# Optimization experiments

Hardware: AMD Instinct MI355X
Metric: run time of the kernel (lower is better)

## Reference

```python
import jax, jax.numpy as jnp
import numpy as np

NTOKENS = 50257
NHID = 1024
NPC = int(np.ceil(np.sqrt(NTOKENS)))            # 225 tokens per class
NCLASSES = int(np.ceil(NTOKENS / NPC))          # 224 classes
BATCH = 1024
INITRANGE = 0.1


def setup_inputs() -> dict:
    key = jax.random.key(0)
    k1, k2, k3, k4 = jax.random.split(key, 4)
    inputs = jax.random.normal(k1, (BATCH, NHID), dtype=jnp.float32)
    labels = jax.random.randint(k2, (BATCH,), 0, NTOKENS, dtype=jnp.int64)
    layer_top_W = jax.random.uniform(k3, (NHID, NCLASSES), minval=-INITRANGE, maxval=INITRANGE, dtype=jnp.float32)
    layer_top_b = jnp.zeros((NCLASSES,), dtype=jnp.float32)
    layer_bottom_W = jax.random.uniform(k4, (NCLASSES, NHID, NPC), minval=-INITRANGE, maxval=INITRANGE, dtype=jnp.float32)
    layer_bottom_b = jnp.zeros((NCLASSES, NPC), dtype=jnp.float32)
    return {
        "inputs": inputs,
        "labels": labels,
        "layer_top_W": layer_top_W,
        "layer_top_b": layer_top_b,
        "layer_bottom_W": layer_bottom_W,
        "layer_bottom_b": layer_bottom_b,
    }


def reference(inputs, labels, layer_top_W, layer_top_b, layer_bottom_W, layer_bottom_b):
    batch_size = inputs.shape[0]
    # decompose label into (class, within-class) position; old-torch `/` on Long == floor div
    pos_top = labels // NPC            # [B]
    pos_bottom = labels % NPC          # [B]

    # top-level class distribution: [B, nclasses]
    top_logits = inputs @ layer_top_W + layer_top_b
    top_probs = jax.nn.softmax(top_logits, axis=1)

    # gather per-sample class weight slices and do batched matvec:
    # layer_bottom_W[pos_top]: [B, nhid, npc]
    bottom_logits = jnp.einsum("bd,bdc->bc", inputs, layer_bottom_W[pos_top]) + layer_bottom_b[pos_top]
    bottom_probs = jax.nn.softmax(bottom_logits, axis=1)

    rows = jnp.arange(batch_size)
    target_probs = top_probs[rows, pos_top] * bottom_probs[rows, pos_bottom]  # [B]
    return target_probs
```

## Files before the change

### kernel.cpp

```cpp
#include <hip/hip_runtime.h>
#include <math.h>

#define NHID 1024
#define NPC  225
#define NCLS 224
#define BATCH 1024

#define MAX_ITEMS 352
#define N_TOP     (BATCH / 8)
#define GRID_SZ   (1 + N_TOP + MAX_ITEMS)

#define WS_NITEMS 0
#define WS_ORDER  16
#define WS_ITEMS  2048
#define WS_PTOP   4096
#define WS_DONE   6144

#define NITEMS_TAG 0x5A5A0000
#define DONE_MAGIC 0x5A5A5A5A

__device__ __forceinline__ void st_rlx(int* p, int v) {
    __hip_atomic_store(p, v, __ATOMIC_RELAXED, __HIP_MEMORY_SCOPE_AGENT);
}
__device__ __forceinline__ int ld_rlx(int* p) {
    return __hip_atomic_load(p, __ATOMIC_RELAXED, __HIP_MEMORY_SCOPE_AGENT);
}

__global__ __launch_bounds__(512, 4) void hs_fused(
    const float* __restrict__ X, const int* __restrict__ labels,
    const float* __restrict__ Wt, const float* __restrict__ bt,
    const float* __restrict__ Wb, const float* __restrict__ bb,
    int* __restrict__ ws, float* __restrict__ out)
{
    __shared__ __align__(16) float sm[12288];
    __shared__ int s_n;
    const int tid  = threadIdx.x;
    const int bid  = blockIdx.x;
    const int wave = tid >> 6;
    const int lane = tid & 63;

    if (bid == 0) {
        int* cnt   = (int*)sm;
        int* scan  = (int*)sm + 256;
        int* iscan = (int*)sm + 512;
        int* cur   = (int*)sm + 768;
        if (tid < 256) cnt[tid] = 0;
        __syncthreads();
        for (int i = tid; i < BATCH; i += 512)
            atomicAdd(&cnt[labels[i] / NPC], 1);
        __syncthreads();
        int myc = 0, myi = 0;
        if (tid < 256) {
            myc = (tid < NCLS) ? cnt[tid] : 0;
            myi = (myc + 7) >> 3;
            scan[tid] = myc; iscan[tid] = myi;
        }
        __syncthreads();
        for (int off = 1; off < 256; off <<= 1) {
            int a = 0, b = 0;
            if (tid < 256 && tid >= off) { a = scan[tid - off]; b = iscan[tid - off]; }
            __syncthreads();
            if (tid < 256) { scan[tid] += a; iscan[tid] += b; }
            __syncthreads();
        }
        if (tid < 256) {
            const int sbase = scan[tid] - myc;
            const int ibase = iscan[tid] - myi;
            cur[tid] = sbase;
            if (tid < NCLS) {
                for (int t = 0; t < myi; ++t) {
                    int* it = ws + WS_ITEMS + 4 * (ibase + t);
                    st_rlx(it + 0, tid);
                    st_rlx(it + 1, sbase + 8 * t);
                    st_rlx(it + 2, min(8, myc - 8 * t));
                }
            }
        }
        __syncthreads();
        for (int i = tid; i < BATCH; i += 512) {
            int c = labels[i] / NPC;
            int p = atomicAdd(&cur[c], 1);
            st_rlx(ws + WS_ORDER + p, i);
        }
        __syncthreads();
        if (tid == 0)
            __hip_atomic_store(ws + WS_NITEMS, NITEMS_TAG | iscan[255],
                               __ATOMIC_RELEASE, __HIP_MEMORY_SCOPE_AGENT);
        return;
    }

    if (bid <= N_TOP) {
        const int sbase = (bid - 1) * 8;
        for (int idx = tid; idx < 2048; idx += 512) {
            const int j  = idx >> 8;
            const int d4 = idx & 255;
            const float4 v = ((const float4*)&X[(size_t)(sbase + j) * NHID])[d4];
            sm[(4 * d4 + 0) * 12 + j] = v.x;
            sm[(4 * d4 + 1) * 12 + j] = v.y;
            sm[(4 * d4 + 2) * 12 + j] = v.z;
            sm[(4 * d4 + 3) * 12 + j] = v.w;
        }
        __syncthreads();

        float acc[8][4];
#pragma unroll
        for (int j = 0; j < 8; ++j)
#pragma unroll
            for (int k = 0; k < 4; ++k) acc[j][k] = 0.f;

        const int c0 = lane, c1 = lane + 64, c2 = lane + 128, c3 = lane + 192;
        const bool m3 = (c3 < NCLS);
        const int d0 = wave * 128;
        const float* Wr = Wt + (size_t)d0 * NCLS;

        auto ldrow = [&](int r, float* o) {
            const float* p = Wr + (size_t)r * NCLS;
            o[0] = p[c0]; o[1] = p[c1]; o[2] = p[c2];
            o[3] = m3 ? p[c3] : 0.f;
        };
        float wbuf[4][4];
        ldrow(0, wbuf[0]); ldrow(1, wbuf[1]); ldrow(2, wbuf[2]); ldrow(3, wbuf[3]);

#pragma unroll 4
        for (int dd = 0; dd < 128; ++dd) {
            const int slot = dd & 3;
            const float cw0 = wbuf[slot][0], cw1 = wbuf[slot][1],
                        cw2 = wbuf[slot][2], cw3 = wbuf[slot][3];
            ldrow(min(dd + 4, 127), wbuf[slot]);
            const float4 a = *(const float4*)&sm[(d0 + dd) * 12 + 0];
            const float4 b = *(const float4*)&sm[(d0 + dd) * 12 + 4];
            const float xi[8] = {a.x, a.y, a.z, a.w, b.x, b.y, b.z, b.w};
#pragma unroll
            for (int j = 0; j < 8; ++j) {
                acc[j][0] = fmaf(xi[j], cw0, acc[j][0]);
                acc[j][1] = fmaf(xi[j], cw1, acc[j][1]);
                acc[j][2] = fmaf(xi[j], cw2, acc[j][2]);
                acc[j][3] = fmaf(xi[j], cw3, acc[j][3]);
            }
        }
        __syncthreads();

        float* red = sm;
        if (wave >= 4) {
#pragma unroll
            for (int j = 0; j < 8; ++j)
#pragma unroll
                for (int k = 0; k < 4; ++k) {
                    int c = lane + 64 * k;
                    if (c < NCLS) red[((wave - 4) * 8 + j) * 232 + c] = acc[j][k];
                }
        }
        __syncthreads();
        if (wave < 4) {
#pragma unroll
            for (int j = 0; j < 8; ++j)
#pragma unroll
                for (int k = 0; k < 4; ++k) {
                    int c = lane + 64 * k;
                    if (c < NCLS) red[(wave * 8 + j) * 232 + c] += acc[j][k];
                }
        }
        __syncthreads();

        {
            const int j = wave;
            const int s = sbase + j;
            float v[4];
#pragma unroll
            for (int k = 0; k < 4; ++k) {
                int c = lane + 64 * k;
                v[k] = (c < NCLS)
                         ? (red[(0 * 8 + j) * 232 + c] + red[(1 * 8 + j) * 232 + c] +
                            red[(2 * 8 + j) * 232 + c] + red[(3 * 8 + j) * 232 + c] +
                            bt[c])
                         : -INFINITY;
            }
            float m = fmaxf(fmaxf(v[0], v[1]), fmaxf(v[2], v[3]));
            for (int o = 32; o > 0; o >>= 1) m = fmaxf(m, __shfl_xor(m, o));
            float e = expf(v[0] - m) + expf(v[1] - m) + expf(v[2] - m) + expf(v[3] - m);
            for (int o = 32; o > 0; o >>= 1) e += __shfl_xor(e, o);
            const int pt = labels[s] / NPC;
            if (lane == (pt & 63))
                st_rlx(ws + WS_PTOP + s, __float_as_int(expf(v[pt >> 6] - m) / e));
        }
        __syncthreads();
        if (tid == 0)
            __hip_atomic_store(ws + WS_DONE + (bid - 1), DONE_MAGIC,
                               __ATOMIC_RELEASE, __HIP_MEMORY_SCOPE_AGENT);
        return;
    }

    if (tid == 0) {
        int dv;
        for (;;) {
            dv = __hip_atomic_load(ws + WS_NITEMS, __ATOMIC_ACQUIRE,
                                   __HIP_MEMORY_SCOPE_AGENT);
            if ((dv & 0xFFFF0000) == NITEMS_TAG) break;
            __builtin_amdgcn_s_sleep(8);
        }
        s_n = dv & 0xFFFF;
    }
    __syncthreads();
    const int bi = bid - 1 - N_TOP;
    if (bi >= s_n) return;

    int* it = ws + WS_ITEMS + 4 * bi;
    const int cls = ld_rlx(it + 0);
    const int s0  = ld_rlx(it + 1);
    const int nt  = ld_rlx(it + 2);

    int s_ids[8];
#pragma unroll
    for (int j = 0; j < 8; ++j)
        s_ids[j] = (j < nt) ? ld_rlx(ws + WS_ORDER + s0 + j) : 0;

    for (int idx = tid; idx < 2048; idx += 512) {
        const int j  = idx >> 8;
        const int d4 = idx & 255;
        float4 v = make_float4(0.f, 0.f, 0.f, 0.f);
        if (j < nt) v = ((const float4*)&X[(size_t)s_ids[j] * NHID])[d4];
        sm[(4 * d4 + 0) * 12 + j] = v.x;
        sm[(4 * d4 + 1) * 12 + j] = v.y;
        sm[(4 * d4 + 2) * 12 + j] = v.z;
        sm[(4 * d4 + 3) * 12 + j] = v.w;
    }
    __syncthreads();

    float acc[8][4];
#pragma unroll
    for (int j = 0; j < 8; ++j)
#pragma unroll
        for (int k = 0; k < 4; ++k) acc[j][k] = 0.f;

    const int c0 = lane, c1 = lane + 64, c2 = lane + 128, c3 = lane + 192;
    const bool m3 = (c3 < NPC);
    const int d0 = wave * 128;
    const float* Wr = Wb + (size_t)cls * (NHID * NPC) + (size_t)d0 * NPC;

    auto ldrow = [&](int r, float* o) {
        const float* p = Wr + (size_t)r * NPC;
        o[0] = __builtin_nontemporal_load(p + c0);
        o[1] = __builtin_nontemporal_load(p + c1);
        o[2] = __builtin_nontemporal_load(p + c2);
        o[3] = m3 ? __builtin_nontemporal_load(p + c3) : 0.f;
    };
    float wbuf[4][4];
    ldrow(0, wbuf[0]); ldrow(1, wbuf[1]); ldrow(2, wbuf[2]); ldrow(3, wbuf[3]);

#pragma unroll 4
    for (int dd = 0; dd < 128; ++dd) {
        const int slot = dd & 3;
        const float cw0 = wbuf[slot][0], cw1 = wbuf[slot][1],
                    cw2 = wbuf[slot][2], cw3 = wbuf[slot][3];
        ldrow(min(dd + 4, 127), wbuf[slot]);
        const float4 a = *(const float4*)&sm[(d0 + dd) * 12 + 0];
        const float4 b = *(const float4*)&sm[(d0 + dd) * 12 + 4];
        const float xi[8] = {a.x, a.y, a.z, a.w, b.x, b.y, b.z, b.w};
#pragma unroll
        for (int j = 0; j < 8; ++j) {
            acc[j][0] = fmaf(xi[j], cw0, acc[j][0]);
            acc[j][1] = fmaf(xi[j], cw1, acc[j][1]);
            acc[j][2] = fmaf(xi[j], cw2, acc[j][2]);
            acc[j][3] = fmaf(xi[j], cw3, acc[j][3]);
        }
    }
    __syncthreads();

    float* red = sm;
    if (wave >= 4) {
#pragma unroll
        for (int j = 0; j < 8; ++j)
#pragma unroll
            for (int k = 0; k < 4; ++k) {
                int c = lane + 64 * k;
                if (c < NPC) red[((wave - 4) * 8 + j) * 232 + c] = acc[j][k];
            }
    }
    __syncthreads();
    if (wave < 4) {
#pragma unroll
        for (int j = 0; j < 8; ++j)
#pragma unroll
            for (int k = 0; k < 4; ++k) {
                int c = lane + 64 * k;
                if (c < NPC) red[(wave * 8 + j) * 232 + c] += acc[j][k];
            }
    }
    __syncthreads();

    {
        const int j = wave;
        if (j < nt) {
            const int s = s_ids[j];
            float v[4];
#pragma unroll
            for (int k = 0; k < 4; ++k) {
                int c = lane + 64 * k;
                v[k] = (c < NPC)
                         ? (red[(0 * 8 + j) * 232 + c] + red[(1 * 8 + j) * 232 + c] +
                            red[(2 * 8 + j) * 232 + c] + red[(3 * 8 + j) * 232 + c] +
                            bb[(size_t)cls * NPC + c])
                         : -INFINITY;
            }
            float m = fmaxf(fmaxf(v[0], v[1]), fmaxf(v[2], v[3]));
            for (int o = 32; o > 0; o >>= 1) m = fmaxf(m, __shfl_xor(m, o));
            float e = expf(v[0] - m) + expf(v[1] - m) + expf(v[2] - m) + expf(v[3] - m);
            for (int o = 32; o > 0; o >>= 1) e += __shfl_xor(e, o);
            const int pb = labels[s] % NPC;
            if (lane == (pb & 63)) {
                int dv;
                for (;;) {
                    dv = __hip_atomic_load(ws + WS_DONE + (s >> 3), __ATOMIC_ACQUIRE,
                                           __HIP_MEMORY_SCOPE_AGENT);
                    if (dv == DONE_MAGIC) break;
                    __builtin_amdgcn_s_sleep(8);
                }
                const float pt = __int_as_float(ld_rlx(ws + WS_PTOP + s));
                out[s] = pt * (expf(v[pb >> 6] - m) / e);
            }
        }
    }
}

extern "C" void kernel_launch(void* const* d_in, const int* in_sizes, int n_in,
                              void* d_out, int out_size, void* d_ws, size_t ws_size,
                              hipStream_t stream)
{
    const float* X      = (const float*)d_in[0];
    const int*   labels = (const int*)  d_in[1];
    const float* Wt     = (const float*)d_in[2];
    const float* bt     = (const float*)d_in[3];
    const float* Wb     = (const float*)d_in[4];
    const float* bb     = (const float*)d_in[5];

    hipLaunchKernelGGL(hs_fused, dim3(GRID_SZ), dim3(512), 0, stream,
                       X, labels, Wt, bt, Wb, bb, (int*)d_ws, (float*)d_out);
}
```

Measured before the change: 325.1 us.

## Split fused kernel into two launches and widen blocks to 1024 threads

Replaces the single persistent-style kernel, which used spin-wait flags between grouping, top-softmax and bottom blocks, with two stream-ordered kernels: one for grouping plus the top softmax, one for the bottom softmax. Blocks grow to 1024 threads, so each wave covers 64 hidden dims instead of 128, followed by an 8-way shared-memory reduction. The X transpose store pattern also changes. This removes the atomic polling and sleep loops, in exchange for a second launch and a hard barrier that stops the bottom work from overlapping with the top work.

```diff
diff --git a/kernel.cpp b/kernel.cpp
--- a/kernel.cpp
+++ b/kernel.cpp
@@ -8,221 +8,203 @@
 
 #define MAX_ITEMS 352
 #define N_TOP     (BATCH / 8)
-#define GRID_SZ   (1 + N_TOP + MAX_ITEMS)
 
 #define WS_NITEMS 0
 #define WS_ORDER  16
 #define WS_ITEMS  2048
 #define WS_PTOP   4096
-#define WS_DONE   6144
-
-#define NITEMS_TAG 0x5A5A0000
-#define DONE_MAGIC 0x5A5A5A5A
-
-__device__ __forceinline__ void st_rlx(int* p, int v) {
-    __hip_atomic_store(p, v, __ATOMIC_RELAXED, __HIP_MEMORY_SCOPE_AGENT);
+
+__device__ __forceinline__ void group_samples(const int* __restrict__ labels,
+                                              int* __restrict__ ws,
+                                              float* __restrict__ smf, int tid)
+{
+    int* cnt   = (int*)smf;
+    int* scan  = (int*)smf + 256;
+    int* iscan = (int*)smf + 512;
+    int* cur   = (int*)smf + 768;
+
+    if (tid < 256) cnt[tid] = 0;
+    __syncthreads();
+    for (int i = tid; i < BATCH; i += 1024)
+        atomicAdd(&cnt[labels[i] / NPC], 1);
+    __syncthreads();
+
+    int myc = 0, myi = 0;
+    if (tid < 256) {
+        myc = (tid < NCLS) ? cnt[tid] : 0;
+        myi = (myc + 7) >> 3;
+        scan[tid]  = myc;
+        iscan[tid] = myi;
+    }
+    __syncthreads();
+    for (int off = 1; off < 256; off <<= 1) {
+        int a = 0, b = 0;
+        if (tid < 256 && tid >= off) { a = scan[tid - off]; b = iscan[tid - off]; }
+        __syncthreads();
+        if (tid < 256) { scan[tid] += a; iscan[tid] += b; }
+        __syncthreads();
+    }
+    if (tid < 256) {
+        const int sbase = scan[tid]  - myc;
+        const int ibase = iscan[tid] - myi;
+        if (tid == 255) ws[WS_NITEMS] = iscan[255];
+        cur[tid] = sbase;
+        if (tid < NCLS) {
+            for (int t = 0; t < myi; ++t) {
+                int* it = ws + WS_ITEMS + 4 * (ibase + t);
+                it[0] = tid;
+                it[1] = sbase + 8 * t;
+                it[2] = min(8, myc - 8 * t);
+            }
+        }
+    }
+    __syncthreads();
+    for (int i = tid; i < BATCH; i += 1024) {
+        int c = labels[i] / NPC;
+        int p = atomicAdd(&cur[c], 1);
+        ws[WS_ORDER + p] = i;
+    }
 }
-__device__ __forceinline__ int ld_rlx(int* p) {
-    return __hip_atomic_load(p, __ATOMIC_RELAXED, __HIP_MEMORY_SCOPE_AGENT);
-}
-
-__global__ __launch_bounds__(512, 4) void hs_fused(
-    const float* __restrict__ X, const int* __restrict__ labels,
-    const float* __restrict__ Wt, const float* __restrict__ bt,
-    const float* __restrict__ Wb, const float* __restrict__ bb,
-    int* __restrict__ ws, float* __restrict__ out)
+
+__global__ __launch_bounds__(1024, 4) void k1_top(const float* __restrict__ X,
+                                                  const int* __restrict__ labels,
+                                                  const float* __restrict__ Wt,
+                                                  const float* __restrict__ bt,
+                                                  int* __restrict__ ws)
 {
-    __shared__ __align__(16) float sm[12288];
-    __shared__ int s_n;
+    __shared__ __align__(16) float sm[14848];
     const int tid  = threadIdx.x;
-    const int bid  = blockIdx.x;
     const int wave = tid >> 6;
     const int lane = tid & 63;
 
-    if (bid == 0) {
-        int* cnt   = (int*)sm;
-        int* scan  = (int*)sm + 256;
-        int* iscan = (int*)sm + 512;
-        int* cur   = (int*)sm + 768;
-        if (tid < 256) cnt[tid] = 0;
-        __syncthreads();
-        for (int i = tid; i < BATCH; i += 512)
-            atomicAdd(&cnt[labels[i] / NPC], 1);
-        __syncthreads();
-        int myc = 0, myi = 0;
-        if (tid < 256) {
-            myc = (tid < NCLS) ? cnt[tid] : 0;
-            myi = (myc + 7) >> 3;
-            scan[tid] = myc; iscan[tid] = myi;
-        }
-        __syncthreads();
-        for (int off = 1; off < 256; off <<= 1) {
-            int a = 0, b = 0;
-            if (tid < 256 && tid >= off) { a = scan[tid - off]; b = iscan[tid - off]; }
-            __syncthreads();
-            if (tid < 256) { scan[tid] += a; iscan[tid] += b; }
-            __syncthreads();
-        }
-        if (tid < 256) {
-            const int sbase = scan[tid] - myc;
-            const int ibase = iscan[tid] - myi;
-            cur[tid] = sbase;
-            if (tid < NCLS) {
-                for (int t = 0; t < myi; ++t) {
-                    int* it = ws + WS_ITEMS + 4 * (ibase + t);
-                    st_rlx(it + 0, tid);
-                    st_rlx(it + 1, sbase + 8 * t);
-                    st_rlx(it + 2, min(8, myc - 8 * t));
-                }
-            }
-        }
-        __syncthreads();
-        for (int i = tid; i < BATCH; i += 512) {
-            int c = labels[i] / NPC;
-            int p = atomicAdd(&cur[c], 1);
-            st_rlx(ws + WS_ORDER + p, i);
-        }
-        __syncthreads();
-        if (tid == 0)
-            __hip_atomic_store(ws + WS_NITEMS, NITEMS_TAG | iscan[255],
-                               __ATOMIC_RELEASE, __HIP_MEMORY_SCOPE_AGENT);
+    if (blockIdx.x == N_TOP) {
+        group_samples(labels, ws, sm, tid);
         return;
     }
-
-    if (bid <= N_TOP) {
-        const int sbase = (bid - 1) * 8;
-        for (int idx = tid; idx < 2048; idx += 512) {
-            const int j  = idx >> 8;
-            const int d4 = idx & 255;
-            const float4 v = ((const float4*)&X[(size_t)(sbase + j) * NHID])[d4];
-            sm[(4 * d4 + 0) * 12 + j] = v.x;
-            sm[(4 * d4 + 1) * 12 + j] = v.y;
-            sm[(4 * d4 + 2) * 12 + j] = v.z;
-            sm[(4 * d4 + 3) * 12 + j] = v.w;
-        }
-        __syncthreads();
-
-        float acc[8][4];
+    const int sbase = blockIdx.x * 8;
+
+    for (int idx = tid; idx < 2048; idx += 1024) {
+        const int j  = idx & 7;
+        const int d4 = idx >> 3;
+        const float4 v = ((const float4*)&X[(size_t)(sbase + j) * NHID])[d4];
+        float* p = &sm[48 * d4 + j];
+        p[0] = v.x; p[12] = v.y; p[24] = v.z; p[36] = v.w;
+    }
+    __syncthreads();
+
+    float acc[8][4];
+#pragma unroll
+    for (int j = 0; j < 8; ++j)
+#pragma unroll
+        for (int k = 0; k < 4; ++k) acc[j][k] = 0.f;
+
+    const int c0 = lane, c1 = lane + 64, c2 = lane + 128, c3 = lane + 192;
+    const bool m3 = (c3 < NCLS);
+    const int d0 = wave * 64;
+    const float* Wr = Wt + (size_t)d0 * NCLS;
+
+    auto ldrow = [&](int r, float* o) {
+        const float* p = Wr + (size_t)r * NCLS;
+        o[0] = p[c0]; o[1] = p[c1]; o[2] = p[c2];
+        o[3] = m3 ? p[c3] : 0.f;
+    };
+    float wbuf[4][4];
+    ldrow(0, wbuf[0]); ldrow(1, wbuf[1]); ldrow(2, wbuf[2]); ldrow(3, wbuf[3]);
+
+#pragma unroll 4
+    for (int dd = 0; dd < 64; ++dd) {
+        const int slot = dd & 3;
+        const float cw0 = wbuf[slot][0], cw1 = wbuf[slot][1],
+                    cw2 = wbuf[slot][2], cw3 = wbuf[slot][3];
+        ldrow(min(dd + 4, 63), wbuf[slot]);
+        const float4 a = *(const float4*)&sm[(d0 + dd) * 12 + 0];
+        const float4 b = *(const float4*)&sm[(d0 + dd) * 12 + 4];
+        const float xi[8] = {a.x, a.y, a.z, a.w, b.x, b.y, b.z, b.w};
+#pragma unroll
+        for (int j = 0; j < 8; ++j) {
+            acc[j][0] = fmaf(xi[j], cw0, acc[j][0]);
+            acc[j][1] = fmaf(xi[j], cw1, acc[j][1]);
+            acc[j][2] = fmaf(xi[j], cw2, acc[j][2]);
+            acc[j][3] = fmaf(xi[j], cw3, acc[j][3]);
+        }
+    }
+    __syncthreads();
+
+    float* red = sm;
+    if (wave >= 8) {
 #pragma unroll
         for (int j = 0; j < 8; ++j)
 #pragma unroll
-            for (int k = 0; k < 4; ++k) acc[j][k] = 0.f;
-
-        const int c0 = lane, c1 = lane + 64, c2 = lane + 128, c3 = lane + 192;
-        const bool m3 = (c3 < NCLS);
-        const int d0 = wave * 128;
-        const float* Wr = Wt + (size_t)d0 * NCLS;
-
-        auto ldrow = [&](int r, float* o) {
-            const float* p = Wr + (size_t)r * NCLS;
-            o[0] = p[c0]; o[1] = p[c1]; o[2] = p[c2];
-            o[3] = m3 ? p[c3] : 0.f;
-        };
-        float wbuf[4][4];
-        ldrow(0, wbuf[0]); ldrow(1, wbuf[1]); ldrow(2, wbuf[2]); ldrow(3, wbuf[3]);
-
-#pragma unroll 4
-        for (int dd = 0; dd < 128; ++dd) {
-            const int slot = dd & 3;
-            const float cw0 = wbuf[slot][0], cw1 = wbuf[slot][1],
-                        cw2 = wbuf[slot][2], cw3 = wbuf[slot][3];
-            ldrow(min(dd + 4, 127), wbuf[slot]);
-            const float4 a = *(const float4*)&sm[(d0 + dd) * 12 + 0];
-            const float4 b = *(const float4*)&sm[(d0 + dd) * 12 + 4];
-            const float xi[8] = {a.x, a.y, a.z, a.w, b.x, b.y, b.z, b.w};
-#pragma unroll
-            for (int j = 0; j < 8; ++j) {
-                acc[j][0] = fmaf(xi[j], cw0, acc[j][0]);
-                acc[j][1] = fmaf(xi[j], cw1, acc[j][1]);
-                acc[j][2] = fmaf(xi[j], cw2, acc[j][2]);
-                acc[j][3] = fmaf(xi[j], cw3, acc[j][3]);
-            }
-        }
-        __syncthreads();
-
-        float* red = sm;
-        if (wave >= 4) {
-#pragma unroll
-            for (int j = 0; j < 8; ++j)
-#pragma unroll
-                for (int k = 0; k < 4; ++k) {
-                    int c = lane + 64 * k;
-                    if (c < NCLS) red[((wave - 4) * 8 + j) * 232 + c] = acc[j][k];
-                }
-        }
-        __syncthreads();
-        if (wave < 4) {
-#pragma unroll
-            for (int j = 0; j < 8; ++j)
-#pragma unroll
-                for (int k = 0; k < 4; ++k) {
-                    int c = lane + 64 * k;
-                    if (c < NCLS) red[(wave * 8 + j) * 232 + c] += acc[j][k];
-                }
-        }
-        __syncthreads();
-
-        {
-            const int j = wave;
-            const int s = sbase + j;
-            float v[4];
-#pragma unroll
-            for (int k = 0; k < 4; ++k) {
-                int c = lane + 64 * k;
-                v[k] = (c < NCLS)
-                         ? (red[(0 * 8 + j) * 232 + c] + red[(1 * 8 + j) * 232 + c] +
-                            red[(2 * 8 + j) * 232 + c] + red[(3 * 8 + j) * 232 + c] +
-                            bt[c])
-                         : -INFINITY;
-            }
-            float m = fmaxf(fmaxf(v[0], v[1]), fmaxf(v[2], v[3]));
-            for (int o = 32; o > 0; o >>= 1) m = fmaxf(m, __shfl_xor(m, o));
-            float e = expf(v[0] - m) + expf(v[1] - m) + expf(v[2] - m) + expf(v[3] - m);
-            for (int o = 32; o > 0; o >>= 1) e += __shfl_xor(e, o);
-            const int pt = labels[s] / NPC;
-            if (lane == (pt & 63))
-                st_rlx(ws + WS_PTOP + s, __float_as_int(expf(v[pt >> 6] - m) / e));
-        }
-        __syncthreads();
-        if (tid == 0)
-            __hip_atomic_store(ws + WS_DONE + (bid - 1), DONE_MAGIC,
-                               __ATOMIC_RELEASE, __HIP_MEMORY_SCOPE_AGENT);
-        return;
-    }
-
-    if (tid == 0) {
-        int dv;
-        for (;;) {
-            dv = __hip_atomic_load(ws + WS_NITEMS, __ATOMIC_ACQUIRE,
-                                   __HIP_MEMORY_SCOPE_AGENT);
-            if ((dv & 0xFFFF0000) == NITEMS_TAG) break;
-            __builtin_amdgcn_s_sleep(8);
-        }
-        s_n = dv & 0xFFFF;
-    }
-    __syncthreads();
-    const int bi = bid - 1 - N_TOP;
-    if (bi >= s_n) return;
-
-    int* it = ws + WS_ITEMS + 4 * bi;
-    const int cls = ld_rlx(it + 0);
-    const int s0  = ld_rlx(it + 1);
-    const int nt  = ld_rlx(it + 2);
+            for (int k = 0; k < 4; ++k) {
+                int c = lane + 64 * k;
+                if (c < NCLS) red[((wave - 8) * 8 + j) * 232 + c] = acc[j][k];
+            }
+    }
+    __syncthreads();
+    if (wave < 8) {
+#pragma unroll
+        for (int j = 0; j < 8; ++j)
+#pragma unroll
+            for (int k = 0; k < 4; ++k) {
+                int c = lane + 64 * k;
+                if (c < NCLS) red[(wave * 8 + j) * 232 + c] += acc[j][k];
+            }
+    }
+    __syncthreads();
+
+    if (wave < 8) {
+        const int j = wave;
+        const int s = sbase + j;
+        float v[4];
+#pragma unroll
+        for (int k = 0; k < 4; ++k) {
+            int c = lane + 64 * k;
+            if (c < NCLS) {
+                float t = bt[c];
+#pragma unroll
+                for (int g = 0; g < 8; ++g) t += red[(g * 8 + j) * 232 + c];
+                v[k] = t;
+            } else v[k] = -INFINITY;
+        }
+        float m = fmaxf(fmaxf(v[0], v[1]), fmaxf(v[2], v[3]));
+        for (int o = 32; o > 0; o >>= 1) m = fmaxf(m, __shfl_xor(m, o));
+        float e = expf(v[0] - m) + expf(v[1] - m) + expf(v[2] - m) + expf(v[3] - m);
+        for (int o = 32; o > 0; o >>= 1) e += __shfl_xor(e, o);
+        const int pt = labels[s] / NPC;
+        if (lane == (pt & 63))
+            ((float*)(ws + WS_PTOP))[s] = expf(v[pt >> 6] - m) / e;
+    }
+}
+
+__global__ __launch_bounds__(1024, 4) void k2_bottom(const float* __restrict__ X,
+                                                     const int* __restrict__ labels,
+                                                     const float* __restrict__ Wb,
+                                                     const float* __restrict__ bb,
+                                                     const int* __restrict__ ws,
+                                                     float* __restrict__ out)
+{
+    __shared__ __align__(16) float sm[14848];
+    const int nitems = ws[WS_NITEMS];
+    if ((int)blockIdx.x >= nitems) return;
+    const int* it = ws + WS_ITEMS + 4 * blockIdx.x;
+    const int cls = it[0], s0 = it[1], nt = it[2];
+
+    const int tid  = threadIdx.x;
+    const int wave = tid >> 6;
+    const int lane = tid & 63;
 
     int s_ids[8];
 #pragma unroll
     for (int j = 0; j < 8; ++j)
-        s_ids[j] = (j < nt) ? ld_rlx(ws + WS_ORDER + s0 + j) : 0;
-
-    for (int idx = tid; idx < 2048; idx += 512) {
-        const int j  = idx >> 8;
-        const int d4 = idx & 255;
+        s_ids[j] = (j < nt) ? ws[WS_ORDER + s0 + j] : 0;
+
+    for (int idx = tid; idx < 2048; idx += 1024) {
+        const int j  = idx & 7;
+        const int d4 = idx >> 3;
         float4 v = make_float4(0.f, 0.f, 0.f, 0.f);
         if (j < nt) v = ((const float4*)&X[(size_t)s_ids[j] * NHID])[d4];
-        sm[(4 * d4 + 0) * 12 + j] = v.x;
-        sm[(4 * d4 + 1) * 12 + j] = v.y;
-        sm[(4 * d4 + 2) * 12 + j] = v.z;
-        sm[(4 * d4 + 3) * 12 + j] = v.w;
+        float* p = &sm[48 * d4 + j];
+        p[0] = v.x; p[12] = v.y; p[24] = v.z; p[36] = v.w;
     }
     __syncthreads();
 
@@ -234,7 +216,7 @@
 
     const int c0 = lane, c1 = lane + 64, c2 = lane + 128, c3 = lane + 192;
     const bool m3 = (c3 < NPC);
-    const int d0 = wave * 128;
+    const int d0 = wave * 64;
     const float* Wr = Wb + (size_t)cls * (NHID * NPC) + (size_t)d0 * NPC;
 
     auto ldrow = [&](int r, float* o) {
@@ -248,11 +230,11 @@
     ldrow(0, wbuf[0]); ldrow(1, wbuf[1]); ldrow(2, wbuf[2]); ldrow(3, wbuf[3]);
 
 #pragma unroll 4
-    for (int dd = 0; dd < 128; ++dd) {
+    for (int dd = 0; dd < 64; ++dd) {
         const int slot = dd & 3;
         const float cw0 = wbuf[slot][0], cw1 = wbuf[slot][1],
                     cw2 = wbuf[slot][2], cw3 = wbuf[slot][3];
-        ldrow(min(dd + 4, 127), wbuf[slot]);
+        ldrow(min(dd + 4, 63), wbuf[slot]);
         const float4 a = *(const float4*)&sm[(d0 + dd) * 12 + 0];
         const float4 b = *(const float4*)&sm[(d0 + dd) * 12 + 4];
         const float xi[8] = {a.x, a.y, a.z, a.w, b.x, b.y, b.z, b.w};
@@ -267,17 +249,17 @@
     __syncthreads();
 
     float* red = sm;
-    if (wave >= 4) {
+    if (wave >= 8) {
 #pragma unroll
         for (int j = 0; j < 8; ++j)
 #pragma unroll
             for (int k = 0; k < 4; ++k) {
                 int c = lane + 64 * k;
-                if (c < NPC) red[((wave - 4) * 8 + j) * 232 + c] = acc[j][k];
-            }
-    }
-    __syncthreads();
-    if (wave < 4) {
+                if (c < NPC) red[((wave - 8) * 8 + j) * 232 + c] = acc[j][k];
+            }
+    }
+    __syncthreads();
+    if (wave < 8) {
 #pragma unroll
         for (int j = 0; j < 8; ++j)
 #pragma unroll
@@ -288,7 +270,7 @@
     }
     __syncthreads();
 
-    {
+    if (wave < 8) {
         const int j = wave;
         if (j < nt) {
             const int s = s_ids[j];
@@ -296,11 +278,12 @@
 #pragma unroll
             for (int k = 0; k < 4; ++k) {
                 int c = lane + 64 * k;
-                v[k] = (c < NPC)
-                         ? (red[(0 * 8 + j) * 232 + c] + red[(1 * 8 + j) * 232 + c] +
-                            red[(2 * 8 + j) * 232 + c] + red[(3 * 8 + j) * 232 + c] +
-                            bb[(size_t)cls * NPC + c])
-                         : -INFINITY;
+                if (c < NPC) {
+                    float t = bb[(size_t)cls * NPC + c];
+#pragma unroll
+                    for (int g = 0; g < 8; ++g) t += red[(g * 8 + j) * 232 + c];
+                    v[k] = t;
+                } else v[k] = -INFINITY;
             }
             float m = fmaxf(fmaxf(v[0], v[1]), fmaxf(v[2], v[3]));
             for (int o = 32; o > 0; o >>= 1) m = fmaxf(m, __shfl_xor(m, o));
@@ -308,14 +291,7 @@
             for (int o = 32; o > 0; o >>= 1) e += __shfl_xor(e, o);
             const int pb = labels[s] % NPC;
             if (lane == (pb & 63)) {
-                int dv;
-                for (;;) {
-                    dv = __hip_atomic_load(ws + WS_DONE + (s >> 3), __ATOMIC_ACQUIRE,
-                                           __HIP_MEMORY_SCOPE_AGENT);
-                    if (dv == DONE_MAGIC) break;
-                    __builtin_amdgcn_s_sleep(8);
-                }
-                const float pt = __int_as_float(ld_rlx(ws + WS_PTOP + s));
+                const float pt = ((const float*)(ws + WS_PTOP))[s];
                 out[s] = pt * (expf(v[pb >> 6] - m) / e);
             }
         }
@@ -333,6 +309,8 @@
     const float* Wb     = (const float*)d_in[4];
     const float* bb     = (const float*)d_in[5];
 
-    hipLaunchKernelGGL(hs_fused, dim3(GRID_SZ), dim3(512), 0, stream,
-                       X, labels, Wt, bt, Wb, bb, (int*)d_ws, (float*)d_out);
+    hipLaunchKernelGGL(k1_top, dim3(N_TOP + 1), dim3(1024), 0, stream,
+                       X, labels, Wt, bt, (int*)d_ws);
+    hipLaunchKernelGGL(k2_bottom, dim3(MAX_ITEMS), dim3(1024), 0, stream,
+                       X, labels, Wb, bb, (const int*)d_ws, (float*)d_out);
 }
```

New measurement: 305.0 us. -6.2%, faster.
